# Performance work log

Hardware: AMD Instinct MI355X
Metric: run time of the kernel (lower is better)

## Reference

```python
import jax, jax.numpy as jnp
import numpy as np

D_MODEL = 1024
D_K = 64
B, SQ, SK = 4, 4096, 4096
NEG = -1000000000.0


def setup_inputs() -> dict:
    key = jax.random.key(0)
    ks = jax.random.split(key, 10)
    inp = {
        "x_q": jax.random.normal(ks[0], (B, SQ, D_MODEL), jnp.float32),
        "x_k": jax.random.normal(ks[1], (B, SK, D_MODEL), jnp.float32),
        "x_v": jax.random.normal(ks[2], (B, SK, D_MODEL), jnp.float32),
        "mask": jax.random.randint(ks[3], (B, SQ, SK), 0, 2, jnp.int32),
        "Wq": jax.random.normal(ks[4], (D_K, D_MODEL), jnp.float32) * (1.0 / np.sqrt(D_MODEL)),
        "bq": jax.random.normal(ks[5], (D_K,), jnp.float32) * 0.02,
        "Wk": jax.random.normal(ks[6], (D_K, D_MODEL), jnp.float32) * (1.0 / np.sqrt(D_MODEL)),
        "bk": jax.random.normal(ks[7], (D_K,), jnp.float32) * 0.02,
        "Wv": jax.random.normal(ks[8], (D_K, D_MODEL), jnp.float32) * (1.0 / np.sqrt(D_MODEL)),
        "bv": jax.random.normal(ks[9], (D_K,), jnp.float32) * 0.02,
    }
    return inp


def reference(x_q, x_k, x_v, mask, Wq, bq, Wk, bk, Wv, bv):
    # nn.Linear: y = x @ W.T + b
    q = jnp.einsum("bsd,kd->bsk", x_q, Wq) + bq  # [B, Sq, d_k]
    k = jnp.einsum("bsd,kd->bsk", x_k, Wk) + bk  # [B, Sk, d_k]
    v = jnp.einsum("bsd,kd->bsk", x_v, Wv) + bv  # [B, Sk, d_k]
    scaler = jnp.sqrt(jnp.asarray(D_K, dtype=q.dtype))
    score = jnp.einsum("bqk,bsk->bqs", q, k) / scaler  # [B, Sq, Sk]
    # additive mask: -1e9 where mask == 0
    score = score + jnp.where(mask == 0, jnp.asarray(NEG, score.dtype), jnp.asarray(0.0, score.dtype))
    # NOTE: softmax over dim=1 (the query axis), faithful to the source
    attn = jax.nn.softmax(score, axis=1)
    y = jnp.einsum("bqs,bsk->bqk", attn, v)  # [B, Sq, d_k]
    return y
```

## Files before the change

kernel.cpp:

```cpp
#include <hip/hip_runtime.h>
#include <hip/hip_bf16.h>

#define Bsz 4
#define SQ 4096
#define SK 4096
#define DMODEL 1024
#define DKk 64
#define QSPLIT 8

typedef __attribute__((ext_vector_type(8))) short bf8_t;
typedef __attribute__((ext_vector_type(4))) float f4_t;

#define MFMA(a, b, c) __builtin_amdgcn_mfma_f32_16x16x32_bf16((a), (b), (c), 0, 0, 0)

#define OFF_Q    ((size_t)0)
#define OFF_K    ((size_t)(2u << 20))
#define OFF_V    ((size_t)(4u << 20))
#define OFF_VT   ((size_t)(6u << 20))
#define OFF_BITS ((size_t)(8u << 20))
#define OFF_PART ((size_t)(16u << 20))
#define OFF_LINV (OFF_PART + (512u << 10))

__device__ __forceinline__ short f2bf(float f) {
    union { float f; unsigned u; } v; v.f = f;
    return (short)((v.u + 0x7FFFu + ((v.u >> 16) & 1u)) >> 16);
}
__device__ __forceinline__ float bf2f(short h) {
    union { unsigned u; float f; } v; v.u = ((unsigned)(unsigned short)h) << 16;
    return v.f;
}
__device__ __forceinline__ bf8_t cvt8(float4 a, float4 b) {
    union { __hip_bfloat162 h[4]; bf8_t v; } u;
    u.h[0] = __float22bfloat162_rn(float2{a.x, a.y});
    u.h[1] = __float22bfloat162_rn(float2{a.z, a.w});
    u.h[2] = __float22bfloat162_rn(float2{b.x, b.y});
    u.h[3] = __float22bfloat162_rn(float2{b.z, b.w});
    return u.v;
}

__global__ __launch_bounds__(256) void k_proj(
    const float* __restrict__ xq, const float* __restrict__ xk, const float* __restrict__ xv,
    const float* __restrict__ Wq, const float* __restrict__ bq,
    const float* __restrict__ Wk, const float* __restrict__ bk,
    const float* __restrict__ Wv, const float* __restrict__ bv,
    char* __restrict__ ws)
{
    const int t = threadIdx.x, l = t & 63, w = t >> 6;
    const int l15 = l & 15, g = l >> 4;
    const int which = blockIdx.y;
    const float* x    = which == 0 ? xq : (which == 1 ? xk : xv);
    const float* W    = which == 0 ? Wq : (which == 1 ? Wk : Wv);
    const float* bias = which == 0 ? bq : (which == 1 ? bk : bv);
    short* out = (short*)(ws + (which == 0 ? OFF_Q : (which == 1 ? OFF_K : OFF_V)));
    const float scale = (which == 0) ? 0.125f : 1.0f;

    const int row0 = blockIdx.x * 128 + w * 32;

    f4_t acc[2][4];
#pragma unroll
    for (int m = 0; m < 2; ++m)
#pragma unroll
        for (int n = 0; n < 4; ++n) acc[m][n] = f4_t{0.f, 0.f, 0.f, 0.f};

    for (int kc = 0; kc < DMODEL; kc += 32) {
        bf8_t af[2], bfg[4];
#pragma unroll
        for (int m = 0; m < 2; ++m) {
            const float* p = x + (size_t)(row0 + m * 16 + l15) * DMODEL + kc + g * 8;
            af[m] = cvt8(*(const float4*)p, *(const float4*)(p + 4));
        }
#pragma unroll
        for (int n = 0; n < 4; ++n) {
            const float* p = W + (size_t)(n * 16 + l15) * DMODEL + kc + g * 8;
            bfg[n] = cvt8(*(const float4*)p, *(const float4*)(p + 4));
        }
#pragma unroll
        for (int m = 0; m < 2; ++m)
#pragma unroll
            for (int n = 0; n < 4; ++n) acc[m][n] = MFMA(af[m], bfg[n], acc[m][n]);
    }

#pragma unroll
    for (int n = 0; n < 4; ++n) {
        const float bb = bias[n * 16 + l15];
#pragma unroll
        for (int m = 0; m < 2; ++m)
#pragma unroll
            for (int i = 0; i < 4; ++i) {
                const int row = row0 + m * 16 + g * 4 + i;
                out[(size_t)row * DKk + n * 16 + l15] = f2bf((acc[m][n][i] + bb) * scale);
            }
    }
}

__global__ __launch_bounds__(256) void k_pack(const int* __restrict__ m,
                                              unsigned long long* __restrict__ bits)
{
    const int lane = threadIdx.x & 63;
    const long long nW = (long long)gridDim.x * 4;
    const long long N = (long long)Bsz * SQ * SK;
    long long wid = (long long)blockIdx.x * 4 + (threadIdx.x >> 6);
    for (long long base = wid * 256; base < N; base += nW * 256) {
        unsigned long long b0 = __ballot(m[base + lane] != 0);
        unsigned long long b1 = __ballot(m[base + 64 + lane] != 0);
        unsigned long long b2 = __ballot(m[base + 128 + lane] != 0);
        unsigned long long b3 = __ballot(m[base + 192 + lane] != 0);
        if (lane < 4) {
            unsigned long long v = lane == 0 ? b0 : (lane == 1 ? b1 : (lane == 2 ? b2 : b3));
            bits[base / 64 + lane] = v;
        }
    }
}

__global__ __launch_bounds__(256) void k_colsum(
    const short* __restrict__ Q, const short* __restrict__ K,
    const unsigned* __restrict__ bits, float* __restrict__ part)
{
    const int t = threadIdx.x, l = t & 63, w = t >> 6;
    const int l15 = l & 15, g = l >> 4;
    const int b = blockIdx.y, qs = blockIdx.z;
    const int sw = blockIdx.x * 128 + w * 32;

    bf8_t kb[2][2];
#pragma unroll
    for (int n = 0; n < 2; ++n)
#pragma unroll
        for (int ks = 0; ks < 2; ++ks)
            kb[n][ks] = *(const bf8_t*)(K + (size_t)(b * SK + sw + n * 16 + l15) * DKk + ks * 32 + g * 8);

    float cs0 = 0.f, cs1 = 0.f;
    const int q0b = qs * (SQ / QSPLIT);

    for (int qt = 0; qt < SQ / QSPLIT; qt += 64) {
        bf8_t qa[4][2];
#pragma unroll
        for (int m = 0; m < 4; ++m)
#pragma unroll
            for (int ks = 0; ks < 2; ++ks)
                qa[m][ks] = *(const bf8_t*)(Q + (size_t)(b * SQ + q0b + qt + m * 16 + l15) * DKk + ks * 32 + g * 8);

#pragma unroll
        for (int m = 0; m < 4; ++m) {
            f4_t a0 = {0.f, 0.f, 0.f, 0.f}, a1 = {0.f, 0.f, 0.f, 0.f};
            a0 = MFMA(qa[m][0], kb[0][0], a0);
            a0 = MFMA(qa[m][1], kb[0][1], a0);
            a1 = MFMA(qa[m][0], kb[1][0], a1);
            a1 = MFMA(qa[m][1], kb[1][1], a1);
            const int qr = q0b + qt + m * 16 + g * 4;
#pragma unroll
            for (int i = 0; i < 4; ++i) {
                const unsigned word = bits[(size_t)(b * SQ + qr + i) * 128 + (sw >> 5)];
                if ((word >> l15) & 1u)        cs0 += __expf(a0[i]);
                if ((word >> (16 + l15)) & 1u) cs1 += __expf(a1[i]);
            }
        }
    }

    cs0 += __shfl_xor(cs0, 16); cs0 += __shfl_xor(cs0, 32);
    cs1 += __shfl_xor(cs1, 16); cs1 += __shfl_xor(cs1, 32);
    if (l < 16) {
        float* p = part + (size_t)(qs * Bsz + b) * SK + sw;
        p[l15]      = cs0;
        p[16 + l15] = cs1;
    }
}

__global__ void k_linv(const float* __restrict__ part, float* __restrict__ linv)
{
    const int i = blockIdx.x * 256 + threadIdx.x;
    float s = 0.f;
#pragma unroll
    for (int j = 0; j < QSPLIT; ++j) s += part[(size_t)j * (Bsz * SK) + i];
    linv[i] = 1.0f / s;
}

__global__ void k_vscale(const short* __restrict__ V, const float* __restrict__ linv,
                         short* __restrict__ Vt)
{
    const int tg = blockIdx.x * 256 + threadIdx.x;
    const int b = tg >> 15, rem = tg & 32767;
    const int nch = rem >> 12, s = rem & 4095;
    const float li = linv[b * SK + s];
    union { short s[8]; bf8_t v; } u;
    u.v = *(const bf8_t*)(V + (size_t)(b * SK + s) * DKk + nch * 8);
#pragma unroll
    for (int j = 0; j < 8; ++j)
        Vt[(size_t)(b * DKk + nch * 8 + j) * SK + s] = f2bf(bf2f(u.s[j]) * li);
}

__global__ __launch_bounds__(256) void k_attn(
    const short* __restrict__ Q, const short* __restrict__ K, const short* __restrict__ Vt,
    const unsigned* __restrict__ bits, float* __restrict__ out)
{
    __shared__ __align__(16) short VtL[2][64 * 136];
    __shared__ __align__(16) short Pl[4][16 * 136];
    __shared__ __align__(16) float yred[2][1024];

    const int t = threadIdx.x, l = t & 63, w = t >> 6;
    const int l15 = l & 15, g = l >> 4;
    const int b = blockIdx.y;
    const int qsub = w >> 1, sh = w & 1;
    const int qw = blockIdx.x * 32 + qsub * 16;

    bf8_t qa[2];
#pragma unroll
    for (int ks = 0; ks < 2; ++ks)
        qa[ks] = *(const bf8_t*)(Q + (size_t)(b * SQ + qw + l15) * DKk + ks * 32 + g * 8);

    f4_t acc[4];
#pragma unroll
    for (int n = 0; n < 4; ++n) acc[n] = f4_t{0.f, 0.f, 0.f, 0.f};

    for (int tile = 0; tile < 16; ++tile) {
        const int sBase = sh * 2048 + tile * 128;
        __syncthreads();
#pragma unroll
        for (int it = 0; it < 8; ++it) {
            const int flat = t + 256 * it;
            const int half = flat >> 10, n = (flat >> 4) & 63, ch = flat & 15;
            const int s = half * 2048 + tile * 128 + ch * 8;
            *(bf8_t*)&VtL[half][n * 136 + ch * 8] =
                *(const bf8_t*)(Vt + (size_t)(b * DKk + n) * SK + s);
        }
        __syncthreads();

        uint4 mw[4];
#pragma unroll
        for (int i = 0; i < 4; ++i)
            mw[i] = *(const uint4*)(bits + (size_t)(b * SQ + qw + g * 4 + i) * 128 + (sBase >> 5));

#pragma unroll
        for (int nt = 0; nt < 8; ++nt) {
            f4_t s4 = {0.f, 0.f, 0.f, 0.f};
            const short* kp = K + (size_t)(b * SK + sBase + nt * 16 + l15) * DKk + g * 8;
            s4 = MFMA(qa[0], *(const bf8_t*)kp, s4);
            s4 = MFMA(qa[1], *(const bf8_t*)(kp + 32), s4);
            const int wi = nt >> 1, bp = (nt & 1) * 16 + l15;
#pragma unroll
            for (int i = 0; i < 4; ++i) {
                const unsigned word = ((const unsigned*)&mw[i])[wi];
                const float p = ((word >> bp) & 1u) ? __expf(s4[i]) : 0.0f;
                Pl[w][(g * 4 + i) * 136 + nt * 16 + l15] = f2bf(p);
            }
        }

#pragma unroll
        for (int ks2 = 0; ks2 < 4; ++ks2) {
            const bf8_t pa = *(const bf8_t*)&Pl[w][l15 * 136 + ks2 * 32 + g * 8];
#pragma unroll
            for (int n = 0; n < 4; ++n) {
                const bf8_t vb = *(const bf8_t*)&VtL[sh][(n * 16 + l15) * 136 + ks2 * 32 + g * 8];
                acc[n] = MFMA(pa, vb, acc[n]);
            }
        }
    }

    __syncthreads();
    if (sh == 1) {
#pragma unroll
        for (int n = 0; n < 4; ++n) *(f4_t*)&yred[qsub][l * 16 + n * 4] = acc[n];
    }
    __syncthreads();
    if (sh == 0) {
#pragma unroll
        for (int n = 0; n < 4; ++n) {
            const f4_t o = *(const f4_t*)&yred[qsub][l * 16 + n * 4];
#pragma unroll
            for (int i = 0; i < 4; ++i)
                out[(size_t)(b * SQ + qw + g * 4 + i) * DKk + n * 16 + l15] = acc[n][i] + o[i];
        }
    }
}

extern "C" void kernel_launch(void* const* d_in, const int* in_sizes, int n_in,
                              void* d_out, int out_size, void* d_ws, size_t ws_size,
                              hipStream_t stream)
{
    (void)in_sizes; (void)n_in; (void)out_size; (void)ws_size;
    const float* xq = (const float*)d_in[0];
    const float* xk = (const float*)d_in[1];
    const float* xv = (const float*)d_in[2];
    const int*  mask = (const int*)d_in[3];
    const float* Wq = (const float*)d_in[4];
    const float* bq = (const float*)d_in[5];
    const float* Wk = (const float*)d_in[6];
    const float* bk = (const float*)d_in[7];
    const float* Wv = (const float*)d_in[8];
    const float* bv = (const float*)d_in[9];
    float* out = (float*)d_out;
    char* ws = (char*)d_ws;

    short*    Q    = (short*)(ws + OFF_Q);
    short*    Kk   = (short*)(ws + OFF_K);
    short*    V    = (short*)(ws + OFF_V);
    short*    Vt   = (short*)(ws + OFF_VT);
    unsigned* bits = (unsigned*)(ws + OFF_BITS);
    float*    part = (float*)(ws + OFF_PART);
    float*    linv = (float*)(ws + OFF_LINV);

    k_proj<<<dim3(128, 3), dim3(256), 0, stream>>>(xq, xk, xv, Wq, bq, Wk, bk, Wv, bv, ws);
    k_pack<<<dim3(2048), dim3(256), 0, stream>>>(mask, (unsigned long long*)bits);
    k_colsum<<<dim3(SK / 128, Bsz, QSPLIT), dim3(256), 0, stream>>>(Q, Kk, bits, part);
    k_linv<<<dim3((Bsz * SK) / 256), dim3(256), 0, stream>>>(part, linv);
    k_vscale<<<dim3((Bsz * SK * 8) / 256), dim3(256), 0, stream>>>(V, linv, Vt);
    k_attn<<<dim3(SQ / 32, Bsz), dim3(256), 0, stream>>>(Q, Kk, Vt, bits, out);
}
```

Before: 633.9 us.

## Materialize masked exp scores once and replace fused attention with split-K PV matmul

Replaces the mask bit-packing, column-sum and fused attention kernels with one score kernel. It reads the int mask directly, computes masked exp(QK^T) once, writes it as a bf16 P matrix and emits per-block column sums. A separate split-K kernel multiplies P by the normalized transposed V and accumulates into a pre-zeroed output with atomics. This removes the duplicated QK^T and exp computation, at the cost of writing and rereading a large bf16 score buffer in global memory.

```diff
diff --git a/kernel.cpp b/kernel.cpp
--- a/kernel.cpp
+++ b/kernel.cpp
@@ -6,7 +6,8 @@
 #define SK 4096
 #define DMODEL 1024
 #define DKk 64
-#define QSPLIT 8
+#define QBLKS 16
+#define SSPL 4
 
 typedef __attribute__((ext_vector_type(8))) short bf8_t;
 typedef __attribute__((ext_vector_type(4))) float f4_t;
@@ -14,12 +15,12 @@
 #define MFMA(a, b, c) __builtin_amdgcn_mfma_f32_16x16x32_bf16((a), (b), (c), 0, 0, 0)
 
 #define OFF_Q    ((size_t)0)
-#define OFF_K    ((size_t)(2u << 20))
-#define OFF_V    ((size_t)(4u << 20))
-#define OFF_VT   ((size_t)(6u << 20))
-#define OFF_BITS ((size_t)(8u << 20))
-#define OFF_PART ((size_t)(16u << 20))
-#define OFF_LINV (OFF_PART + (512u << 10))
+#define OFF_K    ((size_t)(2u   << 20))
+#define OFF_V    ((size_t)(4u   << 20))
+#define OFF_VT   ((size_t)(6u   << 20))
+#define OFF_P    ((size_t)(8u   << 20))
+#define OFF_PART ((size_t)(136u << 20))
+#define OFF_LINV ((size_t)(137u << 20))
 
 __device__ __forceinline__ short f2bf(float f) {
     union { float f; unsigned u; } v; v.f = f;
@@ -36,6 +37,11 @@
     u.h[2] = __float22bfloat162_rn(float2{b.x, b.y});
     u.h[3] = __float22bfloat162_rn(float2{b.z, b.w});
     return u.v;
+}
+
+__global__ void k_zero(float4* __restrict__ out)
+{
+    out[blockIdx.x * 256 + threadIdx.x] = float4{0.f, 0.f, 0.f, 0.f};
 }
 
 __global__ __launch_bounds__(256) void k_proj(
@@ -93,85 +99,84 @@
     }
 }
 
-__global__ __launch_bounds__(256) void k_pack(const int* __restrict__ m,
-                                              unsigned long long* __restrict__ bits)
-{
-    const int lane = threadIdx.x & 63;
-    const long long nW = (long long)gridDim.x * 4;
-    const long long N = (long long)Bsz * SQ * SK;
-    long long wid = (long long)blockIdx.x * 4 + (threadIdx.x >> 6);
-    for (long long base = wid * 256; base < N; base += nW * 256) {
-        unsigned long long b0 = __ballot(m[base + lane] != 0);
-        unsigned long long b1 = __ballot(m[base + 64 + lane] != 0);
-        unsigned long long b2 = __ballot(m[base + 128 + lane] != 0);
-        unsigned long long b3 = __ballot(m[base + 192 + lane] != 0);
-        if (lane < 4) {
-            unsigned long long v = lane == 0 ? b0 : (lane == 1 ? b1 : (lane == 2 ? b2 : b3));
-            bits[base / 64 + lane] = v;
-        }
-    }
-}
-
-__global__ __launch_bounds__(256) void k_colsum(
+__global__ __launch_bounds__(256) void k_score(
     const short* __restrict__ Q, const short* __restrict__ K,
-    const unsigned* __restrict__ bits, float* __restrict__ part)
-{
+    const int* __restrict__ mask, short* __restrict__ P, float* __restrict__ part)
+{
+    __shared__ float red[4][64];
     const int t = threadIdx.x, l = t & 63, w = t >> 6;
     const int l15 = l & 15, g = l >> 4;
-    const int b = blockIdx.y, qs = blockIdx.z;
-    const int sw = blockIdx.x * 128 + w * 32;
-
-    bf8_t kb[2][2];
-#pragma unroll
-    for (int n = 0; n < 2; ++n)
+    const int s0 = blockIdx.x * 64;
+    const int b  = blockIdx.z;
+    const int q0 = blockIdx.y * 256 + w * 64;
+
+    bf8_t ka[4][2];
+#pragma unroll
+    for (int m = 0; m < 4; ++m)
 #pragma unroll
         for (int ks = 0; ks < 2; ++ks)
-            kb[n][ks] = *(const bf8_t*)(K + (size_t)(b * SK + sw + n * 16 + l15) * DKk + ks * 32 + g * 8);
-
-    float cs0 = 0.f, cs1 = 0.f;
-    const int q0b = qs * (SQ / QSPLIT);
-
-    for (int qt = 0; qt < SQ / QSPLIT; qt += 64) {
-        bf8_t qa[4][2];
+            ka[m][ks] = *(const bf8_t*)(K + ((size_t)b * SK + s0 + m * 16 + l15) * DKk + ks * 32 + g * 8);
+
+    float cs[4][4];
+#pragma unroll
+    for (int m = 0; m < 4; ++m)
+#pragma unroll
+        for (int i = 0; i < 4; ++i) cs[m][i] = 0.f;
+
+#pragma unroll
+    for (int n = 0; n < 4; ++n) {
+        const size_t qrow = (size_t)b * SQ + q0 + n * 16 + l15;
+        const bf8_t qb0 = *(const bf8_t*)(Q + qrow * DKk + g * 8);
+        const bf8_t qb1 = *(const bf8_t*)(Q + qrow * DKk + 32 + g * 8);
+#pragma unroll
+        for (int m = 0; m < 4; ++m) {
+            f4_t a = {0.f, 0.f, 0.f, 0.f};
+            a = MFMA(ka[m][0], qb0, a);
+            a = MFMA(ka[m][1], qb1, a);
+            const int soff = s0 + m * 16 + g * 4;
+            const int4 mk = *(const int4*)(mask + qrow * SK + soff);
+            const float p0 = mk.x ? __expf(a[0]) : 0.f;
+            const float p1 = mk.y ? __expf(a[1]) : 0.f;
+            const float p2 = mk.z ? __expf(a[2]) : 0.f;
+            const float p3 = mk.w ? __expf(a[3]) : 0.f;
+            cs[m][0] += p0; cs[m][1] += p1; cs[m][2] += p2; cs[m][3] += p3;
+            union { __hip_bfloat162 h[2]; uint2 u2; } pk;
+            pk.h[0] = __float22bfloat162_rn(float2{p0, p1});
+            pk.h[1] = __float22bfloat162_rn(float2{p2, p3});
+            *(uint2*)(P + qrow * SK + soff) = pk.u2;
+        }
+    }
+
+#pragma unroll
+    for (int m = 0; m < 4; ++m)
+#pragma unroll
+        for (int i = 0; i < 4; ++i) {
+            float v = cs[m][i];
+            v += __shfl_xor(v, 1); v += __shfl_xor(v, 2);
+            v += __shfl_xor(v, 4); v += __shfl_xor(v, 8);
+            cs[m][i] = v;
+        }
+    if (l15 == 0) {
 #pragma unroll
         for (int m = 0; m < 4; ++m)
 #pragma unroll
-            for (int ks = 0; ks < 2; ++ks)
-                qa[m][ks] = *(const bf8_t*)(Q + (size_t)(b * SQ + q0b + qt + m * 16 + l15) * DKk + ks * 32 + g * 8);
-
-#pragma unroll
-        for (int m = 0; m < 4; ++m) {
-            f4_t a0 = {0.f, 0.f, 0.f, 0.f}, a1 = {0.f, 0.f, 0.f, 0.f};
-            a0 = MFMA(qa[m][0], kb[0][0], a0);
-            a0 = MFMA(qa[m][1], kb[0][1], a0);
-            a1 = MFMA(qa[m][0], kb[1][0], a1);
-            a1 = MFMA(qa[m][1], kb[1][1], a1);
-            const int qr = q0b + qt + m * 16 + g * 4;
-#pragma unroll
-            for (int i = 0; i < 4; ++i) {
-                const unsigned word = bits[(size_t)(b * SQ + qr + i) * 128 + (sw >> 5)];
-                if ((word >> l15) & 1u)        cs0 += __expf(a0[i]);
-                if ((word >> (16 + l15)) & 1u) cs1 += __expf(a1[i]);
-            }
-        }
-    }
-
-    cs0 += __shfl_xor(cs0, 16); cs0 += __shfl_xor(cs0, 32);
-    cs1 += __shfl_xor(cs1, 16); cs1 += __shfl_xor(cs1, 32);
-    if (l < 16) {
-        float* p = part + (size_t)(qs * Bsz + b) * SK + sw;
-        p[l15]      = cs0;
-        p[16 + l15] = cs1;
+            for (int i = 0; i < 4; ++i) red[w][m * 16 + g * 4 + i] = cs[m][i];
+    }
+    __syncthreads();
+    if (t < 64) {
+        part[((size_t)blockIdx.y * Bsz + b) * SK + s0 + t] =
+            red[0][t] + red[1][t] + red[2][t] + red[3][t];
     }
 }
 
 __global__ void k_linv(const float* __restrict__ part, float* __restrict__ linv)
 {
     const int i = blockIdx.x * 256 + threadIdx.x;
-    float s = 0.f;
-#pragma unroll
-    for (int j = 0; j < QSPLIT; ++j) s += part[(size_t)j * (Bsz * SK) + i];
-    linv[i] = 1.0f / s;
+    const int b = i >> 12, s = i & (SK - 1);
+    float acc = 0.f;
+#pragma unroll
+    for (int j = 0; j < QBLKS; ++j) acc += part[((size_t)j * Bsz + b) * SK + s];
+    linv[i] = 1.0f / acc;
 }
 
 __global__ void k_vscale(const short* __restrict__ V, const float* __restrict__ linv,
@@ -188,88 +193,48 @@
         Vt[(size_t)(b * DKk + nch * 8 + j) * SK + s] = f2bf(bf2f(u.s[j]) * li);
 }
 
-__global__ __launch_bounds__(256) void k_attn(
-    const short* __restrict__ Q, const short* __restrict__ K, const short* __restrict__ Vt,
-    const unsigned* __restrict__ bits, float* __restrict__ out)
-{
-    __shared__ __align__(16) short VtL[2][64 * 136];
-    __shared__ __align__(16) short Pl[4][16 * 136];
-    __shared__ __align__(16) float yred[2][1024];
-
+__global__ __launch_bounds__(256) void k_pv(
+    const short* __restrict__ P, const short* __restrict__ Vt, float* __restrict__ out)
+{
     const int t = threadIdx.x, l = t & 63, w = t >> 6;
     const int l15 = l & 15, g = l >> 4;
-    const int b = blockIdx.y;
-    const int qsub = w >> 1, sh = w & 1;
-    const int qw = blockIdx.x * 32 + qsub * 16;
-
-    bf8_t qa[2];
-#pragma unroll
-    for (int ks = 0; ks < 2; ++ks)
-        qa[ks] = *(const bf8_t*)(Q + (size_t)(b * SQ + qw + l15) * DKk + ks * 32 + g * 8);
-
-    f4_t acc[4];
-#pragma unroll
-    for (int n = 0; n < 4; ++n) acc[n] = f4_t{0.f, 0.f, 0.f, 0.f};
-
-    for (int tile = 0; tile < 16; ++tile) {
-        const int sBase = sh * 2048 + tile * 128;
-        __syncthreads();
-#pragma unroll
-        for (int it = 0; it < 8; ++it) {
-            const int flat = t + 256 * it;
-            const int half = flat >> 10, n = (flat >> 4) & 63, ch = flat & 15;
-            const int s = half * 2048 + tile * 128 + ch * 8;
-            *(bf8_t*)&VtL[half][n * 136 + ch * 8] =
-                *(const bf8_t*)(Vt + (size_t)(b * DKk + n) * SK + s);
-        }
-        __syncthreads();
-
-        uint4 mw[4];
-#pragma unroll
-        for (int i = 0; i < 4; ++i)
-            mw[i] = *(const uint4*)(bits + (size_t)(b * SQ + qw + g * 4 + i) * 128 + (sBase >> 5));
-
-#pragma unroll
-        for (int nt = 0; nt < 8; ++nt) {
-            f4_t s4 = {0.f, 0.f, 0.f, 0.f};
-            const short* kp = K + (size_t)(b * SK + sBase + nt * 16 + l15) * DKk + g * 8;
-            s4 = MFMA(qa[0], *(const bf8_t*)kp, s4);
-            s4 = MFMA(qa[1], *(const bf8_t*)(kp + 32), s4);
-            const int wi = nt >> 1, bp = (nt & 1) * 16 + l15;
-#pragma unroll
-            for (int i = 0; i < 4; ++i) {
-                const unsigned word = ((const unsigned*)&mw[i])[wi];
-                const float p = ((word >> bp) & 1u) ? __expf(s4[i]) : 0.0f;
-                Pl[w][(g * 4 + i) * 136 + nt * 16 + l15] = f2bf(p);
-            }
-        }
-
-#pragma unroll
-        for (int ks2 = 0; ks2 < 4; ++ks2) {
-            const bf8_t pa = *(const bf8_t*)&Pl[w][l15 * 136 + ks2 * 32 + g * 8];
-#pragma unroll
-            for (int n = 0; n < 4; ++n) {
-                const bf8_t vb = *(const bf8_t*)&VtL[sh][(n * 16 + l15) * 136 + ks2 * 32 + g * 8];
-                acc[n] = MFMA(pa, vb, acc[n]);
-            }
-        }
-    }
-
-    __syncthreads();
-    if (sh == 1) {
-#pragma unroll
-        for (int n = 0; n < 4; ++n) *(f4_t*)&yred[qsub][l * 16 + n * 4] = acc[n];
-    }
-    __syncthreads();
-    if (sh == 0) {
-#pragma unroll
-        for (int n = 0; n < 4; ++n) {
-            const f4_t o = *(const f4_t*)&yred[qsub][l * 16 + n * 4];
+    const int b = blockIdx.z;
+    const int qbase = blockIdx.x * 128 + w * 32;
+    const int sbase = blockIdx.y * (SK / SSPL);
+
+    const short* Pb = P + (size_t)b * SQ * SK;
+    const short* Vb = Vt + (size_t)b * DKk * SK;
+
+    f4_t acc[2][4];
+#pragma unroll
+    for (int m = 0; m < 2; ++m)
+#pragma unroll
+        for (int n = 0; n < 4; ++n) acc[m][n] = f4_t{0.f, 0.f, 0.f, 0.f};
+
+#pragma unroll 2
+    for (int it = 0; it < (SK / SSPL) / 32; ++it) {
+        const int s = sbase + it * 32 + g * 8;
+        bf8_t pa[2], vb[4];
+#pragma unroll
+        for (int m = 0; m < 2; ++m)
+            pa[m] = *(const bf8_t*)(Pb + (size_t)(qbase + m * 16 + l15) * SK + s);
+#pragma unroll
+        for (int n = 0; n < 4; ++n)
+            vb[n] = *(const bf8_t*)(Vb + (size_t)(n * 16 + l15) * SK + s);
+#pragma unroll
+        for (int m = 0; m < 2; ++m)
+#pragma unroll
+            for (int n = 0; n < 4; ++n) acc[m][n] = MFMA(pa[m], vb[n], acc[m][n]);
+    }
+
+#pragma unroll
+    for (int m = 0; m < 2; ++m)
+#pragma unroll
+        for (int n = 0; n < 4; ++n)
 #pragma unroll
             for (int i = 0; i < 4; ++i)
-                out[(size_t)(b * SQ + qw + g * 4 + i) * DKk + n * 16 + l15] = acc[n][i] + o[i];
-        }
-    }
+                atomicAdd(out + ((size_t)b * SQ + qbase + m * 16 + g * 4 + i) * DKk + n * 16 + l15,
+                          acc[m][n][i]);
 }
 
 extern "C" void kernel_launch(void* const* d_in, const int* in_sizes, int n_in,
@@ -290,18 +255,18 @@
     float* out = (float*)d_out;
     char* ws = (char*)d_ws;
 
-    short*    Q    = (short*)(ws + OFF_Q);
-    short*    Kk   = (short*)(ws + OFF_K);
-    short*    V    = (short*)(ws + OFF_V);
-    short*    Vt   = (short*)(ws + OFF_VT);
-    unsigned* bits = (unsigned*)(ws + OFF_BITS);
-    float*    part = (float*)(ws + OFF_PART);
-    float*    linv = (float*)(ws + OFF_LINV);
-
+    short* Q    = (short*)(ws + OFF_Q);
+    short* Kk   = (short*)(ws + OFF_K);
+    short* V    = (short*)(ws + OFF_V);
+    short* Vt   = (short*)(ws + OFF_VT);
+    short* P    = (short*)(ws + OFF_P);
+    float* part = (float*)(ws + OFF_PART);
+    float* linv = (float*)(ws + OFF_LINV);
+
+    k_zero<<<dim3((Bsz * SQ * DKk / 4) / 256), dim3(256), 0, stream>>>((float4*)out);
     k_proj<<<dim3(128, 3), dim3(256), 0, stream>>>(xq, xk, xv, Wq, bq, Wk, bk, Wv, bv, ws);
-    k_pack<<<dim3(2048), dim3(256), 0, stream>>>(mask, (unsigned long long*)bits);
-    k_colsum<<<dim3(SK / 128, Bsz, QSPLIT), dim3(256), 0, stream>>>(Q, Kk, bits, part);
+    k_score<<<dim3(SK / 64, SQ / 256, Bsz), dim3(256), 0, stream>>>(Q, Kk, mask, P, part);
     k_linv<<<dim3((Bsz * SK) / 256), dim3(256), 0, stream>>>(part, linv);
     k_vscale<<<dim3((Bsz * SK * 8) / 256), dim3(256), 0, stream>>>(V, linv, Vt);
-    k_attn<<<dim3(SQ / 32, Bsz), dim3(256), 0, stream>>>(Q, Kk, Vt, bits, out);
-}
+    k_pv<<<dim3(SQ / 128, SSPL, Bsz), dim3(256), 0, stream>>>(P, Vt, out);
+}
```

New measurement: 663.9 us. +4.7%, slower.
